# Optimization experiments

Hardware: AMD Instinct MI355X
Metric: run time of the kernel (lower is better)

The kernel has to match this reference:

```python
import jax, jax.numpy as jnp
import numpy as np

N = 100000      # nodes
E = 1250000     # edges
DIN = 128       # in_channels
H = 64          # hidden
DOUT = 40       # out_channels


def setup_inputs() -> dict:
    key = jax.random.key(0)
    k0, k1, k2, k3 = jax.random.split(key, 4)
    x = jax.random.normal(k0, (N, DIN), dtype=jnp.float32)
    edge_index = jax.random.randint(k1, (2, E), 0, N, dtype=jnp.int32)
    # glorot-style init for the GCNConv linear layers
    W1 = jax.random.normal(k2, (DIN, H), dtype=jnp.float32) * np.float32(1.0 / np.sqrt(DIN))
    b1 = jnp.zeros((H,), dtype=jnp.float32)
    W2 = jax.random.normal(k3, (H, DOUT), dtype=jnp.float32) * np.float32(1.0 / np.sqrt(H))
    b2 = jnp.zeros((DOUT,), dtype=jnp.float32)
    return {"x": x, "W1": W1, "b1": b1, "W2": W2, "b2": b2, "edge_index": edge_index}


def reference(x, W1, b1, W2, b2, edge_index):
    # GCN normalization with added self-loops (PyG GCNConv default):
    # norm_e = deg(dst)^-1/2 * deg(src)^-1/2
    loop = jnp.arange(N, dtype=edge_index.dtype)
    src = jnp.concatenate([edge_index[0], loop])
    dst = jnp.concatenate([edge_index[1], loop])
    deg = jax.ops.segment_sum(jnp.ones(src.shape[0], x.dtype), dst, num_segments=N)
    dinv = jax.lax.rsqrt(deg)  # deg >= 1 thanks to self-loops
    norm = dinv[src] * dinv[dst]  # [E+N]

    def gcn_conv(h, W, b):
        h = h @ W                                     # [N, d_out] linear (no bias)
        msg = h[src] * norm[:, None]                  # gather + normalize
        return jax.ops.segment_sum(msg, dst, num_segments=N) + b  # scatter-add + bias

    h = jax.nn.relu(gcn_conv(x, W1, b1))  # dropout p=0.0 -> identity
    return gcn_conv(h, W2, b2)
```

## Files before the change

kernel.cpp:

```cpp
#include <hip/hip_runtime.h>
#include <hip/hip_fp16.h>

#define NN   100000
#define EE   1250000
#define DIN  128
#define HID  64
#define DOUT 40

#define BN   512
#define NB   196
#define CH   4096
#define SEG  8192
#define S_BLKS 306
#define G_BLKS 1563

typedef _Float16 v8h __attribute__((ext_vector_type(8)));
typedef float    v4f __attribute__((ext_vector_type(4)));

__device__ __forceinline__ void acc8(const float4& v, float4& lo, float4& hi) {
    const __half2* hp = (const __half2*)&v;
    float2 f0 = __half22float2(hp[0]), f1 = __half22float2(hp[1]);
    float2 f2 = __half22float2(hp[2]), f3 = __half22float2(hp[3]);
    lo.x += f0.x; lo.y += f0.y; lo.z += f1.x; lo.w += f1.y;
    hi.x += f2.x; hi.y += f2.y; hi.z += f3.x; hi.w += f3.y;
}

__device__ __forceinline__ void fma8(const float4& v, float s, float4& lo, float4& hi) {
    const __half2* hp = (const __half2*)&v;
    float2 f0 = __half22float2(hp[0]), f1 = __half22float2(hp[1]);
    float2 f2 = __half22float2(hp[2]), f3 = __half22float2(hp[3]);
    lo.x += f0.x * s; lo.y += f0.y * s; lo.z += f1.x * s; lo.w += f1.y * s;
    hi.x += f2.x * s; hi.y += f2.y * s; hi.z += f3.x * s; hi.w += f3.y * s;
}

__device__ __forceinline__ void sthalf8(__half* p, const float4& lo, const float4& hi, float d) {
    float4 st;
    __half2* hp = (__half2*)&st;
    hp[0] = __floats2half2_rn(lo.x * d, lo.y * d);
    hp[1] = __floats2half2_rn(lo.z * d, lo.w * d);
    hp[2] = __floats2half2_rn(hi.x * d, hi.y * d);
    hp[3] = __floats2half2_rn(hi.z * d, hi.w * d);
    *(float4*)p = st;
}

__device__ __forceinline__ void load8(const int* __restrict__ esrc, int base, int* e) {
#pragma unroll
    for (int u = 0; u < 8; ++u) e[u] = esrc[base + u];
}

__device__ __forceinline__ void gath8(const float4* __restrict__ tab4, const int* e, int q,
                                      float4* v, int& s) {
#pragma unroll
    for (int u = 0; u < 8; ++u) v[u] = tab4[(size_t)(e[u] & 0x1FFFF) * 8 + q];
    s = 0;
#pragma unroll
    for (int u = 0; u < 8; ++u) s |= ((e[u] >> 17) & 1) << u;
}

__device__ __forceinline__ void unp8(const float4* v, int s,
                                     float4& tl, float4& th, float4& bl, float4& bh) {
#pragma unroll
    for (int u = 0; u < 8; ++u) {
        float su = (float)((s >> u) & 1);
        acc8(v[u], tl, th);
        fma8(v[u], su, bl, bh);
    }
}

__device__ __forceinline__ void agg_span(const float4* __restrict__ tab4,
                                         const int* __restrict__ esrc,
                                         int j, int je, int q,
                                         float4& tl, float4& th, float4& bl, float4& bh) {
    int eA[8], eB[8];
    float4 vA[8], vB[8];
    int sA, sB;
    int n8 = (je - j) >> 3;
    if (n8 > 0) {
        int lastb = j + (n8 - 1) * 8;
        load8(esrc, j, eA);
        gath8(tab4, eA, q, vA, sA);
        if (n8 == 1) {
            unp8(vA, sA, tl, th, bl, bh);
        } else {
            load8(esrc, j + 8, eB);
            int m = 1;
            while (true) {
                load8(esrc, min(j + (m + 1) * 8, lastb), eA);
                gath8(tab4, eB, q, vB, sB);
                unp8(vA, sA, tl, th, bl, bh);
                ++m;
                if (m >= n8) { unp8(vB, sB, tl, th, bl, bh); break; }
                load8(esrc, min(j + (m + 1) * 8, lastb), eB);
                gath8(tab4, eA, q, vA, sA);
                unp8(vB, sB, tl, th, bl, bh);
                ++m;
                if (m >= n8) { unp8(vA, sA, tl, th, bl, bh); break; }
            }
        }
        j += n8 << 3;
    }
    for (; j < je; ++j) {
        int e = esrc[j];
        float4 v = tab4[(size_t)(e & 0x1FFFF) * 8 + q];
        float su = (float)((e >> 17) & 1);
        acc8(v, tl, th);
        fma8(v, su, bl, bh);
    }
}

__global__ __launch_bounds__(256) void k_wprep(const float* __restrict__ W1,
                                               const float* __restrict__ W2,
                                               __half* __restrict__ w1frag,
                                               __half* __restrict__ w2frag,
                                               int* __restrict__ bucket_fill) {
    int t = threadIdx.x;
    if (blockIdx.x == 5 && t < NB) bucket_fill[t] = 0;
    int e = blockIdx.x * 256 + t;
    if (e < 1024) {
        int ct = e >> 8, ki = (e >> 6) & 3, l = e & 63;
        int q = l >> 4, n = l & 15;
        v8h o;
        #pragma unroll
        for (int j = 0; j < 8; ++j)
            o[j] = (_Float16)W1[(ki * 32 + q * 8 + j) * 64 + ct * 16 + n];
        ((v8h*)w1frag)[e] = o;
    } else {
        int e2 = e - 1024;
        if (e2 < 384) {
            int ct = e2 >> 7, ki = (e2 >> 6) & 1, l = e2 & 63;
            int q = l >> 4, n = l & 15;
            int col = ct * 16 + n;
            v8h o;
            #pragma unroll
            for (int j = 0; j < 8; ++j)
                o[j] = (col < DOUT) ? (_Float16)W2[(ki * 32 + q * 8 + j) * DOUT + col]
                                    : (_Float16)0.0f;
            ((v8h*)w2frag)[e2] = o;
        }
    }
}

__global__ __launch_bounds__(256) void k_fat(const int* __restrict__ src,
                                             const int* __restrict__ dst,
                                             int* __restrict__ bucket_fill,
                                             int* __restrict__ ebuf,
                                             const float* __restrict__ x,
                                             const __half* __restrict__ w1frag,
                                             __half* __restrict__ xw1h) {
    __shared__ int smem[4096];
    int t = threadIdx.x;
    if (blockIdx.x < S_BLKS) {
        int* hist  = smem;
        int* gbase = smem + 256;
        int* rcur  = smem + 512;
        for (int i = t; i < NB; i += 256) { hist[i] = 0; rcur[i] = 0; }
        __syncthreads();
        int e0 = blockIdx.x * CH;
        int ep[16], eb[16];
        #pragma unroll
        for (int j = 0; j < 16; ++j) {
            int e = e0 + j * 256 + t;
            bool valid = (e < EE);
            if (valid) {
                int dd_ = dst[e];
                ep[j] = (src[e] << 9) | (dd_ & 511);
                eb[j] = dd_ >> 9;
                atomicAdd(&hist[eb[j]], 1);
            } else {
                ep[j] = 0; eb[j] = -1;
            }
        }
        __syncthreads();
        for (int i = t; i < NB; i += 256)
            gbase[i] = atomicAdd(&bucket_fill[i], hist[i]);
        __syncthreads();
        #pragma unroll
        for (int j = 0; j < 16; ++j) {
            if (eb[j] >= 0) {
                int r = atomicAdd(&rcur[eb[j]], 1);
                ebuf[eb[j] * SEG + gbase[eb[j]] + r] = ep[j];
            }
        }
    } else {
        float4* sb4 = (float4*)smem;
        const float4* wf = (const float4*)w1frag;
        #pragma unroll
        for (int i = 0; i < 4; ++i) sb4[t + i * 256] = wf[t + i * 256];
        __syncthreads();
        const v8h* sbh = (const v8h*)sb4;
        int wv = t >> 6, l = t & 63;
        int q = l >> 4, n = l & 15;
        int row0 = (blockIdx.x - S_BLKS) * 64 + wv * 16;
        int m = row0 + n;
        bool mv = (m < NN);
        const float* xr = x + (size_t)(mv ? m : 0) * DIN + q * 8;
        v8h afrag[4];
        #pragma unroll
        for (int ki = 0; ki < 4; ++ki) {
            float4 u0 = mv ? ((const float4*)(xr + ki * 32))[0] : make_float4(0.f,0.f,0.f,0.f);
            float4 u1 = mv ? ((const float4*)(xr + ki * 32))[1] : make_float4(0.f,0.f,0.f,0.f);
            v8h a;
            a[0] = (_Float16)u0.x; a[1] = (_Float16)u0.y;
            a[2] = (_Float16)u0.z; a[3] = (_Float16)u0.w;
            a[4] = (_Float16)u1.x; a[5] = (_Float16)u1.y;
            a[6] = (_Float16)u1.z; a[7] = (_Float16)u1.w;
            afrag[ki] = a;
        }
        v4f acc[4];
        #pragma unroll
        for (int ct = 0; ct < 4; ++ct) acc[ct] = (v4f){0.f, 0.f, 0.f, 0.f};
        #pragma unroll
        for (int ct = 0; ct < 4; ++ct) {
            #pragma unroll
            for (int ki = 0; ki < 4; ++ki)
                acc[ct] = __builtin_amdgcn_mfma_f32_16x16x32_f16(
                    afrag[ki], sbh[(ct * 4 + ki) * 64 + l], acc[ct], 0, 0, 0);
        }
        _Float16* outh = (_Float16*)xw1h;
        #pragma unroll
        for (int r = 0; r < 4; ++r) {
            int rr = row0 + q * 4 + r;
            if (rr < NN) {
                #pragma unroll
                for (int ct = 0; ct < 4; ++ct)
                    outh[(size_t)rr * HID + ct * 16 + n] = (_Float16)acc[ct][r];
            }
        }
    }
}

__global__ __launch_bounds__(512) void kB_csr(const int* __restrict__ ebuf,
                                              const int* __restrict__ bucket_fill,
                                              int* __restrict__ pofs,
                                              float* __restrict__ dinv,
                                              int* __restrict__ esrc,
                                              __half* __restrict__ xw1h) {
    __shared__ int lcnt[BN], sAa[BN], sBb[BN], lcur[BN];
    int t = threadIdx.x;
    int b = blockIdx.x;
    int eb0 = b * SEG;
    int ecnt = bucket_fill[b];
    lcnt[t] = 0;
    __syncthreads();
    for (int j = t; j < ecnt; j += 512)
        atomicAdd(&lcnt[ebuf[eb0 + j] & 511], 1);
    __syncthreads();
    sAa[t] = lcnt[t];
    __syncthreads();
    int* s = sAa; int* d = sBb;
    for (int off = 1; off < BN; off <<= 1) {
        d[t] = s[t] + ((t >= off) ? s[t - off] : 0);
        __syncthreads();
        int* tmp = s; s = d; d = tmp;
    }
    int base_node = b * BN;
    int excl = s[t] - lcnt[t];
    lcur[t] = excl;
    int node = base_node + t;
    if (node < NN) {
        pofs[node] = ((eb0 + excl) << 10) | lcnt[t];
        dinv[node] = rsqrtf((float)lcnt[t] + 1.0f);
    }
    __syncthreads();
    for (int j = t; j < ecnt; j += 512) {
        int p = ebuf[eb0 + j];
        int r = atomicAdd(&lcur[p & 511], 1);
        esrc[eb0 + r] = (p >> 9) | ((p & 511) << 17);
    }
    float4* xr4 = (float4*)xw1h;
    for (int i = t; i < BN * 8; i += 512) {
        int li = i >> 3;
        int node2 = base_node + li;
        if (node2 < NN) {
            float di = rsqrtf((float)lcnt[li] + 1.0f);
            float4 v = xr4[(size_t)node2 * 8 + (i & 7)];
            __half2* h = (__half2*)&v;
            #pragma unroll
            for (int u = 0; u < 4; ++u) {
                float2 f = __half22float2(h[u]);
                h[u] = __floats2half2_rn(f.x * di, f.y * di);
            }
            xr4[(size_t)node2 * 8 + (i & 7)] = v;
        }
    }
}

__global__ __launch_bounds__(256) void k_fuse(const __half* __restrict__ xw1h,
                                              const float* __restrict__ dinv,
                                              const int* __restrict__ pofs,
                                              const int* __restrict__ esrc,
                                              const float* __restrict__ b1,
                                              const __half* __restrict__ w2frag,
                                              __half* __restrict__ hw2p) {
    __shared__ __half sh[64 * 72];
    __shared__ float4 sb4[384];
    __shared__ float sb1[64];
    int t = threadIdx.x;
    const float4* wf = (const float4*)w2frag;
    if (t < 192) { sb4[t] = wf[t]; sb4[t + 192] = wf[t + 192]; }
    if (t >= 192) sb1[t - 192] = b1[t - 192];

    int d0 = blockIdx.x * 64;
    int g = t >> 3, q = t & 7;
    int dA = d0 + 2 * g;
    const float4* tab4 = (const float4*)xw1h;
    float4 tl = make_float4(0.f,0.f,0.f,0.f), th = make_float4(0.f,0.f,0.f,0.f);
    float4 bl = make_float4(0.f,0.f,0.f,0.f), bh = make_float4(0.f,0.f,0.f,0.f);
    if (dA < NN) {
        int pA_ = pofs[dA], pB_ = pofs[dA + 1];
        int j  = pA_ >> 10;
        int je = (pB_ >> 10) + (pB_ & 1023);
        float4 sA = tab4[(size_t)dA * 8 + q];
        float4 sB = tab4[(size_t)(dA + 1) * 8 + q];
        acc8(sA, tl, th);
        acc8(sB, tl, th);
        acc8(sB, bl, bh);
        agg_span(tab4, esrc, j, je, q, tl, th, bl, bh);
        float diA = dinv[dA], diB = dinv[dA + 1];
        float4 al = make_float4(tl.x - bl.x, tl.y - bl.y, tl.z - bl.z, tl.w - bl.w);
        float4 ah = make_float4(th.x - bh.x, th.y - bh.y, th.z - bh.z, th.w - bh.w);
        sthalf8(sh + (2 * g) * 72 + q * 8, al, ah, diA);
        sthalf8(sh + (2 * g + 1) * 72 + q * 8, bl, bh, diB);
    } else {
        float4 z = make_float4(0.f,0.f,0.f,0.f);
        sthalf8(sh + (2 * g) * 72 + q * 8, z, z, 0.f);
        sthalf8(sh + (2 * g + 1) * 72 + q * 8, z, z, 0.f);
    }
    __syncthreads();

    const v8h* sbh = (const v8h*)sb4;
    int wv = t >> 6, l = t & 63;
    int qq = l >> 4, n = l & 15;
    int srow = wv * 16 + n;
    v8h afrag[2];
    #pragma unroll
    for (int ki = 0; ki < 2; ++ki) {
        v8h a = *(const v8h*)(sh + srow * 72 + ki * 32 + qq * 8);
        #pragma unroll
        for (int jj = 0; jj < 8; ++jj) {
            float av = (float)a[jj] + sb1[ki * 32 + qq * 8 + jj];
            a[jj] = (_Float16)fmaxf(av, 0.f);
        }
        afrag[ki] = a;
    }
    v4f acc[3];
    #pragma unroll
    for (int ct = 0; ct < 3; ++ct) acc[ct] = (v4f){0.f, 0.f, 0.f, 0.f};
    #pragma unroll
    for (int ct = 0; ct < 3; ++ct) {
        #pragma unroll
        for (int ki = 0; ki < 2; ++ki)
            acc[ct] = __builtin_amdgcn_mfma_f32_16x16x32_f16(
                afrag[ki], sbh[(ct * 2 + ki) * 64 + l], acc[ct], 0, 0, 0);
    }
    _Float16* outh = (_Float16*)hw2p;
    #pragma unroll
    for (int r = 0; r < 4; ++r) {
        int rr = d0 + wv * 16 + qq * 4 + r;
        if (rr < NN) {
            float di = dinv[rr];
            #pragma unroll
            for (int ct = 0; ct < 3; ++ct)
                outh[(size_t)rr * 64 + ct * 16 + n] = (_Float16)(acc[ct][r] * di);
        }
    }
}

__global__ __launch_bounds__(256) void k_agg2(const __half* __restrict__ hw2p,
                                              const float* __restrict__ dinv,
                                              const int* __restrict__ pofs,
                                              const int* __restrict__ esrc,
                                              const float* __restrict__ b2,
                                              float* __restrict__ out) {
    int t = threadIdx.x;
    int g = t >> 3, q = t & 7;
    int d0 = blockIdx.x * 64;
    int dA = d0 + 2 * g;
    if (dA >= NN) return;
    const float4* tab4 = (const float4*)hw2p;
    float4 tl = make_float4(0.f,0.f,0.f,0.f), th = make_float4(0.f,0.f,0.f,0.f);
    float4 bl = make_float4(0.f,0.f,0.f,0.f), bh = make_float4(0.f,0.f,0.f,0.f);
    int pA_ = pofs[dA], pB_ = pofs[dA + 1];
    int j  = pA_ >> 10;
    int je = (pB_ >> 10) + (pB_ & 1023);
    float4 sA = tab4[(size_t)dA * 8 + q];
    float4 sB = tab4[(size_t)(dA + 1) * 8 + q];
    acc8(sA, tl, th);
    acc8(sB, tl, th);
    acc8(sB, bl, bh);
    agg_span(tab4, esrc, j, je, q, tl, th, bl, bh);
    if (q < 5) {
        float diA = dinv[dA], diB = dinv[dA + 1];
        const float4* b24 = (const float4*)(b2 + q * 8);
        float4 c0 = b24[0], c1 = b24[1];
        float* opA = out + (size_t)dA * DOUT + q * 8;
        ((float4*)opA)[0] = make_float4((tl.x - bl.x) * diA + c0.x, (tl.y - bl.y) * diA + c0.y,
                                        (tl.z - bl.z) * diA + c0.z, (tl.w - bl.w) * diA + c0.w);
        ((float4*)opA)[1] = make_float4((th.x - bh.x) * diA + c1.x, (th.y - bh.y) * diA + c1.y,
                                        (th.z - bh.z) * diA + c1.z, (th.w - bh.w) * diA + c1.w);
        float* opB = out + (size_t)(dA + 1) * DOUT + q * 8;
        ((float4*)opB)[0] = make_float4(bl.x * diB + c0.x, bl.y * diB + c0.y,
                                        bl.z * diB + c0.z, bl.w * diB + c0.w);
        ((float4*)opB)[1] = make_float4(bh.x * diB + c1.x, bh.y * diB + c1.y,
                                        bh.z * diB + c1.z, bh.w * diB + c1.w);
    }
}

extern "C" void kernel_launch(void* const* d_in, const int* in_sizes, int n_in,
                              void* d_out, int out_size, void* d_ws, size_t ws_size,
                              hipStream_t stream) {
    const float* x  = (const float*)d_in[0];
    const float* W1 = (const float*)d_in[1];
    const float* b1 = (const float*)d_in[2];
    const float* W2 = (const float*)d_in[3];
    const float* b2 = (const float*)d_in[4];
    const int*   ei = (const int*)d_in[5];
    const int* src = ei;
    const int* dst = ei + EE;
    float* out = (float*)d_out;

    float* ws = (float*)d_ws;
    int*    bucket_fill = (int*)ws;
    int*    pofs        = (int*)ws + 256;
    float*  dinv        = ws + 100352;
    int*    ebuf        = (int*)ws + 200704;
    int*    esrc        = (int*)ws + 1806336;
    __half* xw1h        = (__half*)(ws + 3411968);
    __half* hw2p        = (__half*)(ws + 6611968);
    __half* w1frag      = (__half*)(ws + 9811968);
    __half* w2frag      = (__half*)(ws + 9816064);

    k_wprep <<<6, 256, 0, stream>>>(W1, W2, w1frag, w2frag, bucket_fill);
    k_fat   <<<S_BLKS + G_BLKS, 256, 0, stream>>>(src, dst, bucket_fill, ebuf, x, w1frag, xw1h);
    kB_csr  <<<NB, 512, 0, stream>>>(ebuf, bucket_fill, pofs, dinv, esrc, xw1h);
    k_fuse  <<<(NN + 63) / 64, 256, 0, stream>>>(xw1h, dinv, pofs, esrc, b1, w2frag, hw2p);
    k_agg2  <<<(NN + 63) / 64, 256, 0, stream>>>(hw2p, dinv, pofs, esrc, b2, out);
}
```

Measured before the change: 201.9 us.

## Apply source dinv during layer-1 gather and pack layer-2 table to 40 halves

```diff
diff --git a/kernel.cpp b/kernel.cpp
--- a/kernel.cpp
+++ b/kernel.cpp
@@ -48,10 +48,35 @@
     for (int u = 0; u < 8; ++u) e[u] = esrc[base + u];
 }
 
-__device__ __forceinline__ void gath8(const float4* __restrict__ tab4, const int* e, int q,
-                                      float4* v, int& s) {
-#pragma unroll
-    for (int u = 0; u < 8; ++u) v[u] = tab4[(size_t)(e[u] & 0x1FFFF) * 8 + q];
+__device__ __forceinline__ void gath8d(const float4* __restrict__ tab4,
+                                       const float* __restrict__ dinv,
+                                       const int* e, int q, float4* v, float* dv, int& s) {
+#pragma unroll
+    for (int u = 0; u < 8; ++u) {
+        int id = e[u] & 0x1FFFF;
+        v[u] = tab4[(size_t)id * 8 + q];
+        dv[u] = dinv[id];
+    }
+    s = 0;
+#pragma unroll
+    for (int u = 0; u < 8; ++u) s |= ((e[u] >> 17) & 1) << u;
+}
+
+__device__ __forceinline__ void unp8d(const float4* v, const float* dv, int s,
+                                      float4& tl, float4& th, float4& bl, float4& bh) {
+#pragma unroll
+    for (int u = 0; u < 8; ++u) {
+        float d = dv[u];
+        float ds = ((s >> u) & 1) ? d : 0.f;
+        fma8(v[u], d, tl, th);
+        fma8(v[u], ds, bl, bh);
+    }
+}
+
+__device__ __forceinline__ void gath8p(const float4* __restrict__ tab4,
+                                       const int* e, int qc, float4* v, int& s) {
+#pragma unroll
+    for (int u = 0; u < 8; ++u) v[u] = tab4[(size_t)(e[u] & 0x1FFFF) * 5 + qc];
     s = 0;
 #pragma unroll
     for (int u = 0; u < 8; ++u) s |= ((e[u] >> 17) & 1) << u;
@@ -67,10 +92,55 @@
     }
 }
 
-__device__ __forceinline__ void agg_span(const float4* __restrict__ tab4,
-                                         const int* __restrict__ esrc,
-                                         int j, int je, int q,
-                                         float4& tl, float4& th, float4& bl, float4& bh) {
+__device__ __forceinline__ void agg_span1(const float4* __restrict__ tab4,
+                                          const float* __restrict__ dinv,
+                                          const int* __restrict__ esrc,
+                                          int j, int je, int q,
+                                          float4& tl, float4& th, float4& bl, float4& bh) {
+    int eA[8], eB[8];
+    float4 vA[8], vB[8];
+    float dA[8], dB[8];
+    int sA, sB;
+    int n8 = (je - j) >> 3;
+    if (n8 > 0) {
+        int lastb = j + (n8 - 1) * 8;
+        load8(esrc, j, eA);
+        gath8d(tab4, dinv, eA, q, vA, dA, sA);
+        if (n8 == 1) {
+            unp8d(vA, dA, sA, tl, th, bl, bh);
+        } else {
+            load8(esrc, j + 8, eB);
+            int m = 1;
+            while (true) {
+                load8(esrc, min(j + (m + 1) * 8, lastb), eA);
+                gath8d(tab4, dinv, eB, q, vB, dB, sB);
+                unp8d(vA, dA, sA, tl, th, bl, bh);
+                ++m;
+                if (m >= n8) { unp8d(vB, dB, sB, tl, th, bl, bh); break; }
+                load8(esrc, min(j + (m + 1) * 8, lastb), eB);
+                gath8d(tab4, dinv, eA, q, vA, dA, sA);
+                unp8d(vB, dB, sB, tl, th, bl, bh);
+                ++m;
+                if (m >= n8) { unp8d(vA, dA, sA, tl, th, bl, bh); break; }
+            }
+        }
+        j += n8 << 3;
+    }
+    for (; j < je; ++j) {
+        int e = esrc[j];
+        int id = e & 0x1FFFF;
+        float4 v = tab4[(size_t)id * 8 + q];
+        float d = dinv[id];
+        float ds = ((e >> 17) & 1) ? d : 0.f;
+        fma8(v, d, tl, th);
+        fma8(v, ds, bl, bh);
+    }
+}
+
+__device__ __forceinline__ void agg_span2(const float4* __restrict__ tab4,
+                                          const int* __restrict__ esrc,
+                                          int j, int je, int qc,
+                                          float4& tl, float4& th, float4& bl, float4& bh) {
     int eA[8], eB[8];
     float4 vA[8], vB[8];
     int sA, sB;
@@ -78,7 +148,7 @@
     if (n8 > 0) {
         int lastb = j + (n8 - 1) * 8;
         load8(esrc, j, eA);
-        gath8(tab4, eA, q, vA, sA);
+        gath8p(tab4, eA, qc, vA, sA);
         if (n8 == 1) {
             unp8(vA, sA, tl, th, bl, bh);
         } else {
@@ -86,12 +156,12 @@
             int m = 1;
             while (true) {
                 load8(esrc, min(j + (m + 1) * 8, lastb), eA);
-                gath8(tab4, eB, q, vB, sB);
+                gath8p(tab4, eB, qc, vB, sB);
                 unp8(vA, sA, tl, th, bl, bh);
                 ++m;
                 if (m >= n8) { unp8(vB, sB, tl, th, bl, bh); break; }
                 load8(esrc, min(j + (m + 1) * 8, lastb), eB);
-                gath8(tab4, eA, q, vA, sA);
+                gath8p(tab4, eA, qc, vA, sA);
                 unp8(vB, sB, tl, th, bl, bh);
                 ++m;
                 if (m >= n8) { unp8(vA, sA, tl, th, bl, bh); break; }
@@ -101,7 +171,7 @@
     }
     for (; j < je; ++j) {
         int e = esrc[j];
-        float4 v = tab4[(size_t)(e & 0x1FFFF) * 8 + q];
+        float4 v = tab4[(size_t)(e & 0x1FFFF) * 5 + qc];
         float su = (float)((e >> 17) & 1);
         acc8(v, tl, th);
         fma8(v, su, bl, bh);
@@ -233,8 +303,7 @@
                                               const int* __restrict__ bucket_fill,
                                               int* __restrict__ pofs,
                                               float* __restrict__ dinv,
-                                              int* __restrict__ esrc,
-                                              __half* __restrict__ xw1h) {
+                                              int* __restrict__ esrc) {
     __shared__ int lcnt[BN], sAa[BN], sBb[BN], lcur[BN];
     int t = threadIdx.x;
     int b = blockIdx.x;
@@ -267,22 +336,6 @@
         int r = atomicAdd(&lcur[p & 511], 1);
         esrc[eb0 + r] = (p >> 9) | ((p & 511) << 17);
     }
-    float4* xr4 = (float4*)xw1h;
-    for (int i = t; i < BN * 8; i += 512) {
-        int li = i >> 3;
-        int node2 = base_node + li;
-        if (node2 < NN) {
-            float di = rsqrtf((float)lcnt[li] + 1.0f);
-            float4 v = xr4[(size_t)node2 * 8 + (i & 7)];
-            __half2* h = (__half2*)&v;
-            #pragma unroll
-            for (int u = 0; u < 4; ++u) {
-                float2 f = __half22float2(h[u]);
-                h[u] = __floats2half2_rn(f.x * di, f.y * di);
-            }
-            xr4[(size_t)node2 * 8 + (i & 7)] = v;
-        }
-    }
 }
 
 __global__ __launch_bounds__(256) void k_fuse(const __half* __restrict__ xw1h,
@@ -310,13 +363,13 @@
         int pA_ = pofs[dA], pB_ = pofs[dA + 1];
         int j  = pA_ >> 10;
         int je = (pB_ >> 10) + (pB_ & 1023);
+        float diA = dinv[dA], diB = dinv[dA + 1];
         float4 sA = tab4[(size_t)dA * 8 + q];
         float4 sB = tab4[(size_t)(dA + 1) * 8 + q];
-        acc8(sA, tl, th);
-        acc8(sB, tl, th);
-        acc8(sB, bl, bh);
-        agg_span(tab4, esrc, j, je, q, tl, th, bl, bh);
-        float diA = dinv[dA], diB = dinv[dA + 1];
+        fma8(sA, diA, tl, th);
+        fma8(sB, diB, tl, th);
+        fma8(sB, diB, bl, bh);
+        agg_span1(tab4, dinv, esrc, j, je, q, tl, th, bl, bh);
         float4 al = make_float4(tl.x - bl.x, tl.y - bl.y, tl.z - bl.z, tl.w - bl.w);
         float4 ah = make_float4(th.x - bh.x, th.y - bh.y, th.z - bh.z, th.w - bh.w);
         sthalf8(sh + (2 * g) * 72 + q * 8, al, ah, diA);
@@ -359,9 +412,10 @@
         int rr = d0 + wv * 16 + qq * 4 + r;
         if (rr < NN) {
             float di = dinv[rr];
-            #pragma unroll
-            for (int ct = 0; ct < 3; ++ct)
-                outh[(size_t)rr * 64 + ct * 16 + n] = (_Float16)(acc[ct][r] * di);
+            outh[(size_t)rr * 40 + n]      = (_Float16)(acc[0][r] * di);
+            outh[(size_t)rr * 40 + 16 + n] = (_Float16)(acc[1][r] * di);
+            if (n < 8)
+                outh[(size_t)rr * 40 + 32 + n] = (_Float16)(acc[2][r] * di);
         }
     }
 }
@@ -374,6 +428,7 @@
                                               float* __restrict__ out) {
     int t = threadIdx.x;
     int g = t >> 3, q = t & 7;
+    int qc = (q < 5) ? q : (q - 3);
     int d0 = blockIdx.x * 64;
     int dA = d0 + 2 * g;
     if (dA >= NN) return;
@@ -383,12 +438,12 @@
     int pA_ = pofs[dA], pB_ = pofs[dA + 1];
     int j  = pA_ >> 10;
     int je = (pB_ >> 10) + (pB_ & 1023);
-    float4 sA = tab4[(size_t)dA * 8 + q];
-    float4 sB = tab4[(size_t)(dA + 1) * 8 + q];
+    float4 sA = tab4[(size_t)dA * 5 + qc];
+    float4 sB = tab4[(size_t)(dA + 1) * 5 + qc];
     acc8(sA, tl, th);
     acc8(sB, tl, th);
     acc8(sB, bl, bh);
-    agg_span(tab4, esrc, j, je, q, tl, th, bl, bh);
+    agg_span2(tab4, esrc, j, je, qc, tl, th, bl, bh);
     if (q < 5) {
         float diA = dinv[dA], diB = dinv[dA + 1];
         const float4* b24 = (const float4*)(b2 + q * 8);
@@ -432,7 +487,7 @@
 
     k_wprep <<<6, 256, 0, stream>>>(W1, W2, w1frag, w2frag, bucket_fill);
     k_fat   <<<S_BLKS + G_BLKS, 256, 0, stream>>>(src, dst, bucket_fill, ebuf, x, w1frag, xw1h);
-    kB_csr  <<<NB, 512, 0, stream>>>(ebuf, bucket_fill, pofs, dinv, esrc, xw1h);
+    kB_csr  <<<NB, 512, 0, stream>>>(ebuf, bucket_fill, pofs, dinv, esrc);
     k_fuse  <<<(NN + 63) / 64, 256, 0, stream>>>(xw1h, dinv, pofs, esrc, b1, w2frag, hw2p);
     k_agg2  <<<(NN + 63) / 64, 256, 0, stream>>>(hw2p, dinv, pofs, esrc, b2, out);
 }
```

After: 208.1 us. 3.1% more time.

## Pad CSR neighbor lists to multiples of eight with a zero sentinel row

Applied to the files above, without the earlier changes.

```diff
diff --git a/kernel.cpp b/kernel.cpp
--- a/kernel.cpp
+++ b/kernel.cpp
@@ -11,6 +11,7 @@
 #define NB   196
 #define CH   4096
 #define SEG  8192
+#define SEG2 10240
 #define S_BLKS 306
 #define G_BLKS 1563
 
@@ -23,14 +24,6 @@
     float2 f2 = __half22float2(hp[2]), f3 = __half22float2(hp[3]);
     lo.x += f0.x; lo.y += f0.y; lo.z += f1.x; lo.w += f1.y;
     hi.x += f2.x; hi.y += f2.y; hi.z += f3.x; hi.w += f3.y;
-}
-
-__device__ __forceinline__ void fma8(const float4& v, float s, float4& lo, float4& hi) {
-    const __half2* hp = (const __half2*)&v;
-    float2 f0 = __half22float2(hp[0]), f1 = __half22float2(hp[1]);
-    float2 f2 = __half22float2(hp[2]), f3 = __half22float2(hp[3]);
-    lo.x += f0.x * s; lo.y += f0.y * s; lo.z += f1.x * s; lo.w += f1.y * s;
-    hi.x += f2.x * s; hi.y += f2.y * s; hi.z += f3.x * s; hi.w += f3.y * s;
 }
 
 __device__ __forceinline__ void sthalf8(__half* p, const float4& lo, const float4& hi, float d) {
@@ -43,78 +36,20 @@
     *(float4*)p = st;
 }
 
-__device__ __forceinline__ void load8(const int* __restrict__ esrc, int base, int* e) {
-#pragma unroll
-    for (int u = 0; u < 8; ++u) e[u] = esrc[base + u];
-}
-
-__device__ __forceinline__ void gath8(const float4* __restrict__ tab4, const int* e, int q,
-                                      float4* v, int& s) {
-#pragma unroll
-    for (int u = 0; u < 8; ++u) v[u] = tab4[(size_t)(e[u] & 0x1FFFF) * 8 + q];
-    s = 0;
-#pragma unroll
-    for (int u = 0; u < 8; ++u) s |= ((e[u] >> 17) & 1) << u;
-}
-
-__device__ __forceinline__ void unp8(const float4* v, int s,
-                                     float4& tl, float4& th, float4& bl, float4& bh) {
-#pragma unroll
-    for (int u = 0; u < 8; ++u) {
-        float su = (float)((s >> u) & 1);
-        acc8(v[u], tl, th);
-        fma8(v[u], su, bl, bh);
-    }
-}
-
-__device__ __forceinline__ void agg_span(const float4* __restrict__ tab4,
-                                         const int* __restrict__ esrc,
-                                         int j, int je, int q,
-                                         float4& tl, float4& th, float4& bl, float4& bh) {
-    int eA[8], eB[8];
-    float4 vA[8], vB[8];
-    int sA, sB;
-    int n8 = (je - j) >> 3;
-    if (n8 > 0) {
-        int lastb = j + (n8 - 1) * 8;
-        load8(esrc, j, eA);
-        gath8(tab4, eA, q, vA, sA);
-        if (n8 == 1) {
-            unp8(vA, sA, tl, th, bl, bh);
-        } else {
-            load8(esrc, j + 8, eB);
-            int m = 1;
-            while (true) {
-                load8(esrc, min(j + (m + 1) * 8, lastb), eA);
-                gath8(tab4, eB, q, vB, sB);
-                unp8(vA, sA, tl, th, bl, bh);
-                ++m;
-                if (m >= n8) { unp8(vB, sB, tl, th, bl, bh); break; }
-                load8(esrc, min(j + (m + 1) * 8, lastb), eB);
-                gath8(tab4, eA, q, vA, sA);
-                unp8(vB, sB, tl, th, bl, bh);
-                ++m;
-                if (m >= n8) { unp8(vA, sA, tl, th, bl, bh); break; }
-            }
-        }
-        j += n8 << 3;
-    }
-    for (; j < je; ++j) {
-        int e = esrc[j];
-        float4 v = tab4[(size_t)(e & 0x1FFFF) * 8 + q];
-        float su = (float)((e >> 17) & 1);
-        acc8(v, tl, th);
-        fma8(v, su, bl, bh);
-    }
-}
-
 __global__ __launch_bounds__(256) void k_wprep(const float* __restrict__ W1,
                                                const float* __restrict__ W2,
                                                __half* __restrict__ w1frag,
                                                __half* __restrict__ w2frag,
-                                               int* __restrict__ bucket_fill) {
+                                               int* __restrict__ bucket_fill,
+                                               __half* __restrict__ xw1h,
+                                               __half* __restrict__ hw2p) {
     int t = threadIdx.x;
     if (blockIdx.x == 5 && t < NB) bucket_fill[t] = 0;
+    if (blockIdx.x == 0 && t < 13) {
+        float4 z = make_float4(0.f, 0.f, 0.f, 0.f);
+        if (t < 8) ((float4*)(xw1h + (size_t)NN * HID))[t] = z;
+        else       ((float4*)(hw2p + (size_t)NN * 40))[t - 8] = z;
+    }
     int e = blockIdx.x * 256 + t;
     if (e < 1024) {
         int ct = e >> 8, ki = (e >> 6) & 3, l = e & 63;
@@ -239,13 +174,16 @@
     int t = threadIdx.x;
     int b = blockIdx.x;
     int eb0 = b * SEG;
+    int eb2 = b * SEG2;
     int ecnt = bucket_fill[b];
     lcnt[t] = 0;
     __syncthreads();
     for (int j = t; j < ecnt; j += 512)
         atomicAdd(&lcnt[ebuf[eb0 + j] & 511], 1);
     __syncthreads();
-    sAa[t] = lcnt[t];
+    int cnt  = lcnt[t];
+    int pcnt = (cnt + 7) & ~7;
+    sAa[t] = pcnt;
     __syncthreads();
     int* s = sAa; int* d = sBb;
     for (int off = 1; off < BN; off <<= 1) {
@@ -254,18 +192,19 @@
         int* tmp = s; s = d; d = tmp;
     }
     int base_node = b * BN;
-    int excl = s[t] - lcnt[t];
+    int excl = s[t] - pcnt;
     lcur[t] = excl;
     int node = base_node + t;
     if (node < NN) {
-        pofs[node] = ((eb0 + excl) << 10) | lcnt[t];
-        dinv[node] = rsqrtf((float)lcnt[t] + 1.0f);
-    }
+        pofs[node] = ((eb2 + excl) << 10) | pcnt;
+        dinv[node] = rsqrtf((float)cnt + 1.0f);
+    }
+    for (int i = t; i < SEG2; i += 512) esrc[eb2 + i] = NN;
     __syncthreads();
     for (int j = t; j < ecnt; j += 512) {
         int p = ebuf[eb0 + j];
         int r = atomicAdd(&lcur[p & 511], 1);
-        esrc[eb0 + r] = (p >> 9) | ((p & 511) << 17);
+        esrc[eb2 + r] = p >> 9;
     }
     float4* xr4 = (float4*)xw1h;
     for (int i = t; i < BN * 8; i += 512) {
@@ -285,14 +224,14 @@
     }
 }
 
-__global__ __launch_bounds__(256) void k_fuse(const __half* __restrict__ xw1h,
-                                              const float* __restrict__ dinv,
-                                              const int* __restrict__ pofs,
-                                              const int* __restrict__ esrc,
-                                              const float* __restrict__ b1,
-                                              const __half* __restrict__ w2frag,
-                                              __half* __restrict__ hw2p) {
-    __shared__ __half sh[64 * 72];
+__global__ __launch_bounds__(256, 8) void k_fuse(const __half* __restrict__ xw1h,
+                                                 const float* __restrict__ dinv,
+                                                 const int* __restrict__ pofs,
+                                                 const int* __restrict__ esrc,
+                                                 const float* __restrict__ b1,
+                                                 const __half* __restrict__ w2frag,
+                                                 __half* __restrict__ hw2p) {
+    __shared__ __half sh[32 * 72];
     __shared__ float4 sb4[384];
     __shared__ float sb1[64];
     int t = threadIdx.x;
@@ -300,109 +239,102 @@
     if (t < 192) { sb4[t] = wf[t]; sb4[t + 192] = wf[t + 192]; }
     if (t >= 192) sb1[t - 192] = b1[t - 192];
 
-    int d0 = blockIdx.x * 64;
+    int d0 = blockIdx.x * 32;
     int g = t >> 3, q = t & 7;
-    int dA = d0 + 2 * g;
+    int dd = d0 + g;
     const float4* tab4 = (const float4*)xw1h;
     float4 tl = make_float4(0.f,0.f,0.f,0.f), th = make_float4(0.f,0.f,0.f,0.f);
-    float4 bl = make_float4(0.f,0.f,0.f,0.f), bh = make_float4(0.f,0.f,0.f,0.f);
-    if (dA < NN) {
-        int pA_ = pofs[dA], pB_ = pofs[dA + 1];
-        int j  = pA_ >> 10;
-        int je = (pB_ >> 10) + (pB_ & 1023);
-        float4 sA = tab4[(size_t)dA * 8 + q];
-        float4 sB = tab4[(size_t)(dA + 1) * 8 + q];
-        acc8(sA, tl, th);
-        acc8(sB, tl, th);
-        acc8(sB, bl, bh);
-        agg_span(tab4, esrc, j, je, q, tl, th, bl, bh);
-        float diA = dinv[dA], diB = dinv[dA + 1];
-        float4 al = make_float4(tl.x - bl.x, tl.y - bl.y, tl.z - bl.z, tl.w - bl.w);
-        float4 ah = make_float4(th.x - bh.x, th.y - bh.y, th.z - bh.z, th.w - bh.w);
-        sthalf8(sh + (2 * g) * 72 + q * 8, al, ah, diA);
-        sthalf8(sh + (2 * g + 1) * 72 + q * 8, bl, bh, diB);
-    } else {
-        float4 z = make_float4(0.f,0.f,0.f,0.f);
-        sthalf8(sh + (2 * g) * 72 + q * 8, z, z, 0.f);
-        sthalf8(sh + (2 * g + 1) * 72 + q * 8, z, z, 0.f);
-    }
-    __syncthreads();
-
-    const v8h* sbh = (const v8h*)sb4;
+    acc8(tab4[(size_t)dd * 8 + q], tl, th);
+    int p_ = pofs[dd];
+    int j = p_ >> 10;
+    int n8 = (p_ & 1023) >> 3;
+    for (int m = 0; m < n8; ++m, j += 8) {
+        int e[8];
+        float4 v[8];
+        #pragma unroll
+        for (int u = 0; u < 8; ++u) e[u] = esrc[j + u];
+        #pragma unroll
+        for (int u = 0; u < 8; ++u) v[u] = tab4[(size_t)e[u] * 8 + q];
+        #pragma unroll
+        for (int u = 0; u < 8; ++u) acc8(v[u], tl, th);
+    }
+    sthalf8(sh + g * 72 + q * 8, tl, th, dinv[dd]);
+    __syncthreads();
+
     int wv = t >> 6, l = t & 63;
-    int qq = l >> 4, n = l & 15;
-    int srow = wv * 16 + n;
-    v8h afrag[2];
-    #pragma unroll
-    for (int ki = 0; ki < 2; ++ki) {
-        v8h a = *(const v8h*)(sh + srow * 72 + ki * 32 + qq * 8);
-        #pragma unroll
-        for (int jj = 0; jj < 8; ++jj) {
-            float av = (float)a[jj] + sb1[ki * 32 + qq * 8 + jj];
-            a[jj] = (_Float16)fmaxf(av, 0.f);
-        }
-        afrag[ki] = a;
-    }
-    v4f acc[3];
-    #pragma unroll
-    for (int ct = 0; ct < 3; ++ct) acc[ct] = (v4f){0.f, 0.f, 0.f, 0.f};
-    #pragma unroll
-    for (int ct = 0; ct < 3; ++ct) {
-        #pragma unroll
-        for (int ki = 0; ki < 2; ++ki)
-            acc[ct] = __builtin_amdgcn_mfma_f32_16x16x32_f16(
-                afrag[ki], sbh[(ct * 2 + ki) * 64 + l], acc[ct], 0, 0, 0);
-    }
-    _Float16* outh = (_Float16*)hw2p;
-    #pragma unroll
-    for (int r = 0; r < 4; ++r) {
-        int rr = d0 + wv * 16 + qq * 4 + r;
-        if (rr < NN) {
+    if (wv < 2) {
+        const v8h* sbh = (const v8h*)sb4;
+        int qq = l >> 4, n = l & 15;
+        int srow = wv * 16 + n;
+        v8h afrag[2];
+        #pragma unroll
+        for (int ki = 0; ki < 2; ++ki) {
+            v8h a = *(const v8h*)(sh + srow * 72 + ki * 32 + qq * 8);
+            #pragma unroll
+            for (int jj = 0; jj < 8; ++jj) {
+                float av = (float)a[jj] + sb1[ki * 32 + qq * 8 + jj];
+                a[jj] = (_Float16)fmaxf(av, 0.f);
+            }
+            afrag[ki] = a;
+        }
+        v4f acc[3];
+        #pragma unroll
+        for (int ct = 0; ct < 3; ++ct) acc[ct] = (v4f){0.f, 0.f, 0.f, 0.f};
+        #pragma unroll
+        for (int ct = 0; ct < 3; ++ct) {
+            #pragma unroll
+            for (int ki = 0; ki < 2; ++ki)
+                acc[ct] = __builtin_amdgcn_mfma_f32_16x16x32_f16(
+                    afrag[ki], sbh[(ct * 2 + ki) * 64 + l], acc[ct], 0, 0, 0);
+        }
+        _Float16* outh = (_Float16*)hw2p;
+        #pragma unroll
+        for (int r = 0; r < 4; ++r) {
+            int rr = d0 + wv * 16 + qq * 4 + r;
             float di = dinv[rr];
-            #pragma unroll
-            for (int ct = 0; ct < 3; ++ct)
-                outh[(size_t)rr * 64 + ct * 16 + n] = (_Float16)(acc[ct][r] * di);
-        }
-    }
-}
-
-__global__ __launch_bounds__(256) void k_agg2(const __half* __restrict__ hw2p,
-                                              const float* __restrict__ dinv,
-                                              const int* __restrict__ pofs,
-                                              const int* __restrict__ esrc,
-                                              const float* __restrict__ b2,
-                                              float* __restrict__ out) {
+            outh[(size_t)rr * 40 + n]      = (_Float16)(acc[0][r] * di);
+            outh[(size_t)rr * 40 + 16 + n] = (_Float16)(acc[1][r] * di);
+            if (n < 8)
+                outh[(size_t)rr * 40 + 32 + n] = (_Float16)(acc[2][r] * di);
+        }
+    }
+}
+
+__global__ __launch_bounds__(256, 8) void k_agg2(const __half* __restrict__ hw2p,
+                                                 const float* __restrict__ dinv,
+                                                 const int* __restrict__ pofs,
+                                                 const int* __restrict__ esrc,
+                                                 const float* __restrict__ b2,
+                                                 float* __restrict__ out) {
     int t = threadIdx.x;
     int g = t >> 3, q = t & 7;
-    int d0 = blockIdx.x * 64;
-    int dA = d0 + 2 * g;
-    if (dA >= NN) return;
+    int qc = (q < 5) ? q : (q - 3);
+    int dd = blockIdx.x * 32 + g;
     const float4* tab4 = (const float4*)hw2p;
     float4 tl = make_float4(0.f,0.f,0.f,0.f), th = make_float4(0.f,0.f,0.f,0.f);
-    float4 bl = make_float4(0.f,0.f,0.f,0.f), bh = make_float4(0.f,0.f,0.f,0.f);
-    int pA_ = pofs[dA], pB_ = pofs[dA + 1];
-    int j  = pA_ >> 10;
-    int je = (pB_ >> 10) + (pB_ & 1023);
-    float4 sA = tab4[(size_t)dA * 8 + q];
-    float4 sB = tab4[(size_t)(dA + 1) * 8 + q];
-    acc8(sA, tl, th);
-    acc8(sB, tl, th);
-    acc8(sB, bl, bh);
-    agg_span(tab4, esrc, j, je, q, tl, th, bl, bh);
+    acc8(tab4[(size_t)dd * 5 + qc], tl, th);
+    int p_ = pofs[dd];
+    int j = p_ >> 10;
+    int n8 = (p_ & 1023) >> 3;
+    for (int m = 0; m < n8; ++m, j += 8) {
+        int e[8];
+        float4 v[8];
+        #pragma unroll
+        for (int u = 0; u < 8; ++u) e[u] = esrc[j + u];
+        #pragma unroll
+        for (int u = 0; u < 8; ++u) v[u] = tab4[(size_t)e[u] * 5 + qc];
+        #pragma unroll
+        for (int u = 0; u < 8; ++u) acc8(v[u], tl, th);
+    }
     if (q < 5) {
-        float diA = dinv[dA], diB = dinv[dA + 1];
+        float di = dinv[dd];
         const float4* b24 = (const float4*)(b2 + q * 8);
         float4 c0 = b24[0], c1 = b24[1];
-        float* opA = out + (size_t)dA * DOUT + q * 8;
-        ((float4*)opA)[0] = make_float4((tl.x - bl.x) * diA + c0.x, (tl.y - bl.y) * diA + c0.y,
-                                        (tl.z - bl.z) * diA + c0.z, (tl.w - bl.w) * diA + c0.w);
-        ((float4*)opA)[1] = make_float4((th.x - bh.x) * diA + c1.x, (th.y - bh.y) * diA + c1.y,
-                                        (th.z - bh.z) * diA + c1.z, (th.w - bh.w) * diA + c1.w);
-        float* opB = out + (size_t)(dA + 1) * DOUT + q * 8;
-        ((float4*)opB)[0] = make_float4(bl.x * diB + c0.x, bl.y * diB + c0.y,
-                                        bl.z * diB + c0.z, bl.w * diB + c0.w);
-        ((float4*)opB)[1] = make_float4(bh.x * diB + c1.x, bh.y * diB + c1.y,
-                                        bh.z * diB + c1.z, bh.w * diB + c1.w);
+        float* op = out + (size_t)dd * DOUT + q * 8;
+        ((float4*)op)[0] = make_float4(tl.x * di + c0.x, tl.y * di + c0.y,
+                                       tl.z * di + c0.z, tl.w * di + c0.w);
+        ((float4*)op)[1] = make_float4(th.x * di + c1.x, th.y * di + c1.y,
+                                       th.z * di + c1.z, th.w * di + c1.w);
     }
 }
 
@@ -425,14 +357,14 @@
     float*  dinv        = ws + 100352;
     int*    ebuf        = (int*)ws + 200704;
     int*    esrc        = (int*)ws + 1806336;
-    __half* xw1h        = (__half*)(ws + 3411968);
-    __half* hw2p        = (__half*)(ws + 6611968);
-    __half* w1frag      = (__half*)(ws + 9811968);
-    __half* w2frag      = (__half*)(ws + 9816064);
-
-    k_wprep <<<6, 256, 0, stream>>>(W1, W2, w1frag, w2frag, bucket_fill);
+    __half* xw1h        = (__half*)(ws + 3813376);
+    __half* hw2p        = (__half*)(ws + 7013408);
+    __half* w1frag      = (__half*)(ws + 9013428);
+    __half* w2frag      = (__half*)(ws + 9017524);
+
+    k_wprep <<<6, 256, 0, stream>>>(W1, W2, w1frag, w2frag, bucket_fill, xw1h, hw2p);
     k_fat   <<<S_BLKS + G_BLKS, 256, 0, stream>>>(src, dst, bucket_fill, ebuf, x, w1frag, xw1h);
     kB_csr  <<<NB, 512, 0, stream>>>(ebuf, bucket_fill, pofs, dinv, esrc, xw1h);
-    k_fuse  <<<(NN + 63) / 64, 256, 0, stream>>>(xw1h, dinv, pofs, esrc, b1, w2frag, hw2p);
-    k_agg2  <<<(NN + 63) / 64, 256, 0, stream>>>(hw2p, dinv, pofs, esrc, b2, out);
-}
+    k_fuse  <<<NN / 32, 256, 0, stream>>>(xw1h, dinv, pofs, esrc, b1, w2frag, hw2p);
+    k_agg2  <<<NN / 32, 256, 0, stream>>>(hw2p, dinv, pofs, esrc, b2, out);
+}
```

Result: faster. 182.1 us (-9.8%).
